# Performance work log

Measured on AMD Instinct MI355X. Metric: run time of the kernel, lower is better.

Reference implementation:

```python
import jax, jax.numpy as jnp
import numpy as np

B_, S_, D_ = 16, 2048, 256
H_ = 2 * D_          # S4D d_model = 2*hidden
NS = 64              # S4D state size (d_state)


def _layernorm(x, g, b, eps=1e-5):
    m = jnp.mean(x, axis=-1, keepdims=True)
    v = jnp.var(x, axis=-1, keepdims=True)
    return (x - m) * jax.lax.rsqrt(v + eps) * g + b


def setup_inputs() -> dict:
    key = jax.random.key(0)
    ks = jax.random.split(key, 12)
    x = jax.random.normal(ks[0], (B_, S_, D_), jnp.float32)
    # right-padded mask with varied lengths (signal: lengths = sum(mask), count_zeros = S - lengths)
    lengths = jax.random.randint(ks[1], (B_,), S_ // 2, S_ + 1)
    input_mask = (jnp.arange(S_)[None, :] < lengths[:, None]).astype(jnp.float32)
    # S4D (diag, diag-inv init, bilinear disc) parameters
    log_dt = jax.random.uniform(ks[2], (H_,), minval=jnp.log(1e-3), maxval=jnp.log(1e-1))
    log_A_real = jnp.log(0.5 * jnp.ones((H_, NS), jnp.float32))
    a_imag_row = (NS / jnp.pi) * (NS / (2.0 * jnp.arange(NS, dtype=jnp.float32) + 1.0) - 1.0)
    A_imag = jnp.broadcast_to(a_imag_row, (H_, NS)).copy()
    B_re = jnp.ones((H_, NS), jnp.float32)
    B_im = jnp.zeros((H_, NS), jnp.float32)
    C_re = jax.random.normal(ks[3], (H_, NS), jnp.float32) * (0.5 ** 0.5)
    C_im = jax.random.normal(ks[4], (H_, NS), jnp.float32) * (0.5 ** 0.5)
    D_skip = jax.random.normal(ks[5], (H_,), jnp.float32)
    # GLU: Linear(2D, 2D) then GLU -> D
    W_glu = jax.random.normal(ks[6], (2 * D_, 2 * D_), jnp.float32) / np.sqrt(2 * D_)
    b_glu = jnp.zeros((2 * D_,), jnp.float32)
    ln_gamma = jnp.ones((D_,), jnp.float32)
    ln_beta = jnp.zeros((D_,), jnp.float32)
    return {"input": x, "input_mask": input_mask, "log_dt": log_dt, "log_A_real": log_A_real,
            "A_imag": A_imag, "B_re": B_re, "B_im": B_im, "C_re": C_re, "C_im": C_im,
            "D_skip": D_skip, "W_glu": W_glu, "b_glu": b_glu, "ln_gamma": ln_gamma, "ln_beta": ln_beta}


def _s4d(z, log_dt, log_A_real, A_imag, B_re, B_im, C_re, C_im, D_skip):
    # z: [N, S, H] (transposed=False). Diagonal SSM, bilinear discretization, causal FFT conv.
    N, S, H = z.shape
    dt = jnp.exp(log_dt)[:, None]                        # [H,1]
    A = -jnp.exp(log_A_real) + 1j * A_imag               # [H,NS]
    Bc = B_re + 1j * B_im
    Cc = C_re + 1j * C_im
    dtA = dt * A
    dA = (1.0 + dtA / 2.0) / (1.0 - dtA / 2.0)           # bilinear
    Ct = Cc * Bc * dt / (1.0 - dtA / 2.0)                # folded B*C with bilinear dB factor
    # Vandermonde kernel K[h,l] = 2 Re sum_n Ct[h,n] * dA[h,n]^l
    vand = jnp.exp(jnp.log(dA)[:, :, None] * jnp.arange(S, dtype=jnp.float32))  # [H,NS,S] complex
    K = 2.0 * jnp.real(jnp.einsum('hn,hnl->hl', Ct, vand))                       # [H,S]
    L2 = 2 * S
    k_f = jnp.fft.rfft(K, n=L2)                          # [H, L2/2+1]
    x_f = jnp.fft.rfft(z, n=L2, axis=1)                  # [N, L2/2+1, H]
    y = jnp.fft.irfft(x_f * k_f.T[None], n=L2, axis=1)[:, :S, :]
    y = y + z * D_skip
    return jax.nn.gelu(y)                                # S4 block post-SSM activation; final_act=None, dropout=eval


def reference(input, input_mask, log_dt, log_A_real, A_imag, B_re, B_im, C_re, C_im,
              D_skip, W_glu, b_glu, ln_gamma, ln_beta):
    x = input
    N, S, D = x.shape
    res = x
    state = _layernorm(x, ln_gamma, ln_beta)             # prenorm=True
    count_zeros = jnp.sum(1.0 - input_mask, axis=1).astype(jnp.int32)   # [N]
    # reverse(state, cz): out[i] = state[(S-1-i-cz) mod S]  (flip then roll by count_zeros)
    rev_idx = (S - 1 - jnp.arange(S)[None, :] - count_zeros[:, None]) % S  # [N,S]
    reverse_bstate = jnp.take_along_axis(state, rev_idx[..., None], axis=1)
    z = jnp.concatenate([state, reverse_bstate], axis=-1)                 # [N,S,2D]
    z = _s4d(z, log_dt, log_A_real, A_imag, B_re, B_im, C_re, C_im, D_skip)
    fstate = z[..., :D]
    bstate = jnp.take_along_axis(z[..., D:], rev_idx[..., None], axis=1)  # reverse is an involution
    z = jnp.concatenate([fstate, bstate], axis=-1)                        # [N,S,2D]
    g = z @ W_glu + b_glu
    a, b = jnp.split(g, 2, axis=-1)
    out = a * jax.nn.sigmoid(b)                                           # GLU -> [N,S,D]
    out = out + res
    return out
```

## Files before the change

### kernel.cpp

```cpp
#include <hip/hip_runtime.h>
#include <hip/hip_bf16.h>
#include <math.h>

#define B_ 16
#define S_ 2048
#define D_ 256
#define H_ 512
#define NS_ 64
#define N2 4096
#define M_ (B_*S_)
#define XP(i) ((i) + ((i) >> 4))

typedef float f32x4 __attribute__((ext_vector_type(4)));
typedef short bf16x8 __attribute__((ext_vector_type(8)));

__device__ __forceinline__ unsigned short f2bf(float x) {
    __hip_bfloat16 h = __float2bfloat16(x);
    return *reinterpret_cast<unsigned short*>(&h);
}

__device__ __forceinline__ float gelu_f(float y) {
    float u = y + 0.044715f*y*y*y;
    return y / (1.0f + __builtin_exp2f(-2.3022082f * u));
}

__device__ __forceinline__ float cos_rev(float r) { return __builtin_amdgcn_cosf(r); }
__device__ __forceinline__ float sin_rev(float r) { return __builtin_amdgcn_sinf(r); }

template<bool INV, int MODE>
__device__ __forceinline__ void dft16(float* xr, float* xi) {
    const float SGN = INV ? 1.0f : -1.0f;
    constexpr float W16R[4][4] = {
        {1.f, 1.f, 1.f, 1.f},
        {1.f,  0.92387953251128674f,  0.70710678118654757f,  0.38268343236508984f},
        {1.f,  0.70710678118654757f,  0.0f,                 -0.70710678118654746f},
        {1.f,  0.38268343236508984f, -0.70710678118654746f, -0.92387953251128674f}};
    constexpr float W16I[4][4] = {
        {0.f, 0.f, 0.f, 0.f},
        {0.f, -0.38268343236508978f, -0.70710678118654746f, -0.92387953251128674f},
        {0.f, -0.70710678118654746f, -1.0f,                 -0.70710678118654757f},
        {0.f, -0.92387953251128674f, -0.70710678118654757f,  0.38268343236508967f}};
    float tr[16], ti[16];
    #pragma unroll
    for (int n0 = 0; n0 < 4; ++n0) {
        if (MODE == 1) {
            float ar = xr[n0],   ai = xi[n0];
            float br = xr[n0+4], bi = xi[n0+4];
            tr[0*4+n0] = ar + br;        ti[0*4+n0] = ai + bi;
            tr[2*4+n0] = ar - br;        ti[2*4+n0] = ai - bi;
            tr[1*4+n0] = ar - SGN*bi;    ti[1*4+n0] = ai + SGN*br;
            tr[3*4+n0] = ar + SGN*bi;    ti[3*4+n0] = ai - SGN*br;
        } else {
            float ar = xr[n0],    ai = xi[n0];
            float br = xr[n0+4],  bi = xi[n0+4];
            float cr = xr[n0+8],  ci = xi[n0+8];
            float dr = xr[n0+12], di = xi[n0+12];
            float sacr = ar+cr, saci = ai+ci;
            float dacr = ar-cr, daci = ai-ci;
            float sbdr = br+dr, sbdi = bi+di;
            float dbdr = br-dr, dbdi = bi-di;
            tr[0*4+n0] = sacr + sbdr;      ti[0*4+n0] = saci + sbdi;
            tr[2*4+n0] = sacr - sbdr;      ti[2*4+n0] = saci - sbdi;
            tr[1*4+n0] = dacr - SGN*dbdi;  ti[1*4+n0] = daci + SGN*dbdr;
            tr[3*4+n0] = dacr + SGN*dbdi;  ti[3*4+n0] = daci - SGN*dbdr;
        }
    }
    #pragma unroll
    for (int kl = 1; kl < 4; ++kl) {
        #pragma unroll
        for (int n0 = 1; n0 < 4; ++n0) {
            float wr = W16R[kl][n0];
            float wi = INV ? -W16I[kl][n0] : W16I[kl][n0];
            float pr = tr[kl*4+n0], pi = ti[kl*4+n0];
            tr[kl*4+n0] = pr*wr - pi*wi;
            ti[kl*4+n0] = pr*wi + pi*wr;
        }
    }
    #pragma unroll
    for (int kl = 0; kl < 4; ++kl) {
        float ar = tr[kl*4+0], ai = ti[kl*4+0];
        float br = tr[kl*4+1], bi = ti[kl*4+1];
        float cr = tr[kl*4+2], ci = ti[kl*4+2];
        float dr = tr[kl*4+3], di = ti[kl*4+3];
        float sacr = ar+cr, saci = ai+ci;
        float dacr = ar-cr, daci = ai-ci;
        float sbdr = br+dr, sbdi = bi+di;
        float dbdr = br-dr, dbdi = bi-di;
        xr[kl+0]  = sacr + sbdr;      xi[kl+0]  = saci + sbdi;
        xr[kl+4]  = dacr - SGN*dbdi;  xi[kl+4]  = daci + SGN*dbdr;
        if (MODE != 2) {
            xr[kl+8]  = sacr - sbdr;      xi[kl+8]  = saci - sbdi;
            xr[kl+12] = dacr + SGN*dbdi;  xi[kl+12] = daci - SGN*dbdr;
        }
    }
}

__device__ __forceinline__ void cmul(float& xr_, float& xi_, float wr, float wi) {
    float pr = xr_, pi = xi_;
    xr_ = pr*wr - pi*wi;
    xi_ = pr*wi + pi*wr;
}

__device__ __forceinline__ void twiddle_apply(float* xr, float* xi, float w1r, float w1i) {
    float w2r = w1r*w1r - w1i*w1i, w2i = 2.0f*w1r*w1i;
    float w4r = w2r*w2r - w2i*w2i, w4i = 2.0f*w2r*w2i;
    float w8r = w4r*w4r - w4i*w4i, w8i = 2.0f*w4r*w4i;
    float w3r = w2r*w1r - w2i*w1i, w3i = w2r*w1i + w2i*w1r;
    float w5r = w4r*w1r - w4i*w1i, w5i = w4r*w1i + w4i*w1r;
    float w6r = w4r*w2r - w4i*w2i, w6i = w4r*w2i + w4i*w2r;
    float w7r = w4r*w3r - w4i*w3i, w7i = w4r*w3i + w4i*w3r;
    cmul(xr[1],  xi[1],  w1r, w1i);
    cmul(xr[2],  xi[2],  w2r, w2i);
    cmul(xr[3],  xi[3],  w3r, w3i);
    cmul(xr[4],  xi[4],  w4r, w4i);
    cmul(xr[5],  xi[5],  w5r, w5i);
    cmul(xr[6],  xi[6],  w6r, w6i);
    cmul(xr[7],  xi[7],  w7r, w7i);
    cmul(xr[8],  xi[8],  w8r, w8i);
    float wr, wi;
    wr = w8r*w1r - w8i*w1i; wi = w8r*w1i + w8i*w1r; cmul(xr[9],  xi[9],  wr, wi);
    wr = w8r*w2r - w8i*w2i; wi = w8r*w2i + w8i*w2r; cmul(xr[10], xi[10], wr, wi);
    wr = w8r*w3r - w8i*w3i; wi = w8r*w3i + w8i*w3r; cmul(xr[11], xi[11], wr, wi);
    wr = w8r*w4r - w8i*w4i; wi = w8r*w4i + w8i*w4r; cmul(xr[12], xi[12], wr, wi);
    wr = w8r*w5r - w8i*w5i; wi = w8r*w5i + w8i*w5r; cmul(xr[13], xi[13], wr, wi);
    wr = w8r*w6r - w8i*w6i; wi = w8r*w6i + w8i*w6r; cmul(xr[14], xi[14], wr, wi);
    wr = w8r*w7r - w8i*w7i; wi = w8r*w7i + w8i*w7r; cmul(xr[15], xi[15], wr, wi);
}

__device__ __forceinline__ void fft4096_fwd_reg(float* xr, float* xi, float* lre, float* lim, int t) {
    dft16<false, 1>(xr, xi);
    float rv = (float)t * (1.0f/4096.0f);
    float w1r = cos_rev(rv), w1i = -sin_rev(rv);
    twiddle_apply(xr, xi, w1r, w1i);
    #pragma unroll
    for (int k = 0; k < 16; ++k) { int idx = XP(k*256 + t); lre[idx] = xr[k]; lim[idx] = xi[k]; }
    __syncthreads();
    int k1 = t >> 4, n3 = t & 15;
    #pragma unroll
    for (int n2 = 0; n2 < 16; ++n2) {
        int idx = XP(k1*256 + n2*16 + n3);
        xr[n2] = lre[idx]; xi[n2] = lim[idx];
    }
    dft16<false, 0>(xr, xi);
    rv = (float)n3 * (1.0f/256.0f);
    w1r = cos_rev(rv); w1i = -sin_rev(rv);
    twiddle_apply(xr, xi, w1r, w1i);
    __syncthreads();
    #pragma unroll
    for (int k = 0; k < 16; ++k) { int idx = XP(k1*256 + k*16 + n3); lre[idx] = xr[k]; lim[idx] = xi[k]; }
    __syncthreads();
    int k2 = t & 15;
    #pragma unroll
    for (int n3b = 0; n3b < 16; ++n3b) {
        int idx = XP(k1*256 + k2*16 + n3b);
        xr[n3b] = lre[idx]; xi[n3b] = lim[idx];
    }
    dft16<false, 0>(xr, xi);
}

__device__ __forceinline__ void fft4096_inv_reg(float* xr, float* xi, float* lre, float* lim, int t) {
    int k1 = t >> 4, k2 = t & 15;
    dft16<true, 0>(xr, xi);
    float rv = (float)k2 * (1.0f/256.0f);
    float w1r = cos_rev(rv), w1i = sin_rev(rv);
    twiddle_apply(xr, xi, w1r, w1i);
    __syncthreads();
    #pragma unroll
    for (int k = 0; k < 16; ++k) { int idx = XP(k1*256 + k2*16 + k); lre[idx] = xr[k]; lim[idx] = xi[k]; }
    __syncthreads();
    int n3 = t & 15;
    #pragma unroll
    for (int c = 0; c < 16; ++c) {
        int idx = XP(k1*256 + c*16 + n3);
        xr[c] = lre[idx]; xi[c] = lim[idx];
    }
    dft16<true, 0>(xr, xi);
    __syncthreads();
    #pragma unroll
    for (int k = 0; k < 16; ++k) { int idx = XP(k1*256 + k*16 + n3); lre[idx] = xr[k]; lim[idx] = xi[k]; }
    __syncthreads();
    #pragma unroll
    for (int k = 0; k < 16; ++k) {
        int idx = XP(k*256 + t);
        xr[k] = lre[idx]; xi[k] = lim[idx];
    }
    rv = (float)t * (1.0f/4096.0f);
    w1r = cos_rev(rv); w1i = sin_rev(rv);
    twiddle_apply(xr, xi, w1r, w1i);
    dft16<true, 2>(xr, xi);
}

__global__ void count_kernel(const float* __restrict__ mask, int* __restrict__ cz) {
    int b = blockIdx.x;
    int t = threadIdx.x;
    float s = 0.0f;
    for (int j = t; j < S_; j += 256) s += 1.0f - mask[b*S_ + j];
    for (int off = 32; off; off >>= 1) s += __shfl_xor(s, off);
    __shared__ float red[4];
    if ((t & 63) == 0) red[t >> 6] = s;
    __syncthreads();
    if (t == 0) {
        float tot = red[0] + red[1] + red[2] + red[3];
        cz[b] = (int)(tot + 0.5f);
    }
}

__global__ void wprep_kernel(const float* __restrict__ W, unsigned short* __restrict__ Wt) {
    int idx = blockIdx.x * 256 + threadIdx.x;
    int n = idx >> 9, k = idx & 511;
    Wt[idx] = f2bf(W[k*H_ + n]);
}

__global__ __launch_bounds__(256) void kfft_kernel(
        const float* __restrict__ log_dt, const float* __restrict__ log_A_real,
        const float* __restrict__ A_imag,
        const float* __restrict__ B_re, const float* __restrict__ B_im,
        const float* __restrict__ C_re, const float* __restrict__ C_im,
        float4* __restrict__ Kout) {
    int hp = blockIdx.x, t = threadIdx.x;
    int h0 = hp * 2;
    __shared__ float lre[N2 + N2/16];
    __shared__ float lim[N2 + N2/16];
    __shared__ float thrv[2][NS_], lnr2[2][NS_], ctr[2][NS_], cti[2][NS_];
    __shared__ float stpr[2][NS_], stpi[2][NS_];

    if (t < 128) {
        int ch = t >> 6, n = t & 63, h = h0 + ch;
        float dt = expf(log_dt[h]);
        float Ar = -expf(log_A_real[h*NS_ + n]);
        float Ai = A_imag[h*NS_ + n];
        float drr = 1.0f - 0.5f*dt*Ar, dii = -0.5f*dt*Ai;
        float nr = 1.0f + 0.5f*dt*Ar, ni =  0.5f*dt*Ai;
        float den = drr*drr + dii*dii;
        float dAr = (nr*drr + ni*dii) / den;
        float dAi = (ni*drr - nr*dii) / den;
        float cr = C_re[h*NS_+n], ci = C_im[h*NS_+n];
        float br = B_re[h*NS_+n], bi = B_im[h*NS_+n];
        float pr = (cr*br - ci*bi) * dt, pi = (cr*bi + ci*br) * dt;
        float qr = (pr*drr + pi*dii) / den;
        float qi = (pi*drr - pr*dii) / den;
        float trv = atan2f(dAi, dAr) * 0.15915494309189535f;
        float l2  = 0.5f * log2f(dAr*dAr + dAi*dAi);
        thrv[ch][n] = trv; lnr2[ch][n] = l2;
        ctr[ch][n] = qr;   cti[ch][n] = qi;
        float ms = __builtin_exp2f(l2 * 256.0f);
        float rv = trv * 256.0f; rv -= floorf(rv);
        stpr[ch][n] = ms * cos_rev(rv);
        stpi[ch][n] = ms * sin_rev(rv);
    }
    __syncthreads();

    float xr[16], xi[16];
    #pragma unroll
    for (int j = 0; j < 16; ++j) { xr[j] = 0.0f; xi[j] = 0.0f; }

    float tf = (float)t;
    #pragma unroll
    for (int ch = 0; ch < 2; ++ch) {
        for (int n = 0; n < NS_; ++n) {
            float trv = thrv[ch][n], l2 = lnr2[ch][n];
            float f = trv * tf; f -= floorf(f);
            float mag = __builtin_exp2f(l2 * tf);
            float vr = mag * cos_rev(f);
            float vi = mag * sin_rev(f);
            float sr = stpr[ch][n], si = stpi[ch][n];
            float cr = ctr[ch][n],  ci = cti[ch][n];
            #pragma unroll
            for (int j = 0; j < 8; ++j) {
                float contrib = cr*vr - ci*vi;
                if (ch == 0) xr[j] += contrib; else xi[j] += contrib;
                float nvr = vr*sr - vi*si;
                vi = vr*si + vi*sr;
                vr = nvr;
            }
        }
    }
    #pragma unroll
    for (int j = 0; j < 8; ++j) { xr[j] *= 2.0f; xi[j] *= 2.0f; }

    fft4096_fwd_reg(xr, xi, lre, lim, t);

    __syncthreads();
    #pragma unroll
    for (int k = 0; k < 16; ++k) { int idx = XP(k*256 + t); lre[idx] = xr[k]; lim[idx] = xi[k]; }
    __syncthreads();

    const float scale = 1.0f / (float)N2;
    #pragma unroll
    for (int it = 0; it < 16; ++it) {
        int j = 256*it + t;
        int k = (t >> 4) + ((t & 15) << 4) + (it << 8);
        int kc = (N2 - k) & (N2 - 1);
        int j2 = ((kc >> 8) << 8) + ((kc & 15) << 4) + ((kc >> 4) & 15);
        float za = xr[it], zb = xi[it];
        float zc = lre[XP(j2)], zd = lim[XP(j2)];
        float Xr = 0.5f*(za + zc), Xi2 = 0.5f*(zb - zd);
        float Yr = 0.5f*(zb + zd), Yi = 0.5f*(zc - za);
        Kout[(size_t)hp*N2 + j] = make_float4(Xr*scale, Xi2*scale, Yr*scale, Yi*scale);
    }
}

__global__ __launch_bounds__(256) void ln_kernel(
        const float* __restrict__ x, const float* __restrict__ gamma,
        const float* __restrict__ beta, float* __restrict__ zf) {
    int blk = blockIdx.x;
    int b = blk >> 6;
    int s0 = (blk & 63) * 32;
    int t = threadIdx.x;
    int lane = t & 63, wave = t >> 6;
    __shared__ float st[32][257];

    float4 g4  = *(const float4*)(gamma + lane*4);
    float4 be4 = *(const float4*)(beta  + lane*4);
    for (int q = 0; q < 8; ++q) {
        int row = wave*8 + q;
        int s = s0 + row;
        float4 v = *(const float4*)(x + ((size_t)(b*S_ + s))*D_ + lane*4);
        float sum = v.x + v.y + v.z + v.w;
        float ss  = v.x*v.x + v.y*v.y + v.z*v.z + v.w*v.w;
        for (int off = 32; off; off >>= 1) {
            sum += __shfl_xor(sum, off);
            ss  += __shfl_xor(ss, off);
        }
        float mean = sum * (1.0f/(float)D_);
        float var  = ss  * (1.0f/(float)D_) - mean*mean;
        float rstd = rsqrtf(var + 1e-5f);
        st[row][lane*4+0] = (v.x - mean)*rstd*g4.x + be4.x;
        st[row][lane*4+1] = (v.y - mean)*rstd*g4.y + be4.y;
        st[row][lane*4+2] = (v.z - mean)*rstd*g4.z + be4.z;
        st[row][lane*4+3] = (v.w - mean)*rstd*g4.w + be4.w;
    }
    __syncthreads();
    int s_off = t & 31, dg = t >> 5;
    int s = s0 + s_off;
    for (int i = 0; i < 32; ++i) {
        int d = dg + 8*i;
        zf[((size_t)(b*D_ + d))*S_ + s] = st[s_off][d];
    }
}

__global__ __launch_bounds__(256) void fftconv_kernel(
        const float* __restrict__ zf, const float4* __restrict__ Kf4,
        const float* __restrict__ D_skip, const int* __restrict__ cz,
        unsigned short* __restrict__ ybf) {
    int blk = blockIdx.x;
    int b  = blk >> 8;
    int hp = blk & 255;
    int h0 = hp * 2;
    int t = threadIdx.x;
    __shared__ float lre[N2 + N2/16];
    __shared__ float lim[N2 + N2/16];

    bool back = (h0 >= D_);
    int czb = cz[b];
    const float* zrow1 = zf + ((size_t)(b*D_ + (h0 & (D_-1))))*S_;
    const float* zrow2 = zrow1 + S_;

    float xr[16], xi[16];
    float z1r[8], z2r[8];
    #pragma unroll
    for (int j = 0; j < 8; ++j) {
        int s = t + 256*j;
        int p = s;
        if (back) { p = 2*S_ - 1 - czb - s; if (p >= S_) p -= S_; }
        float v1 = zrow1[p], v2 = zrow2[p];
        z1r[j] = v1; z2r[j] = v2;
        xr[j] = v1;  xi[j] = v2;
        xr[j+8] = 0.0f; xi[j+8] = 0.0f;
    }

    fft4096_fwd_reg(xr, xi, lre, lim, t);

    __syncthreads();
    #pragma unroll
    for (int k = 0; k < 16; ++k) { int idx = XP(k*256 + t); lre[idx] = xr[k]; lim[idx] = xi[k]; }
    __syncthreads();

    const float4* kp = Kf4 + (size_t)hp * N2;
    #pragma unroll
    for (int it = 0; it < 16; ++it) {
        int j = 256*it + t;
        int k = (t >> 4) + ((t & 15) << 4) + (it << 8);
        int kc = (N2 - k) & (N2 - 1);
        int j2 = ((kc >> 8) << 8) + ((kc & 15) << 4) + ((kc >> 4) & 15);
        float za = xr[it], zb = xi[it];
        float zc = lre[XP(j2)], zd = lim[XP(j2)];
        float Xr = 0.5f*(za + zc), Xi2 = 0.5f*(zb - zd);
        float Yr = 0.5f*(zb + zd), Yi = 0.5f*(zc - za);
        float4 kk = kp[j];
        float Pr = Xr*kk.x - Xi2*kk.y, Pi = Xr*kk.y + Xi2*kk.x;
        float Qr = Yr*kk.z - Yi*kk.w,  Qi = Yr*kk.w + Yi*kk.z;
        xr[it] = Pr - Qi;
        xi[it] = Pi + Qr;
    }

    fft4096_inv_reg(xr, xi, lre, lim, t);

    float dsk1 = D_skip[h0], dsk2 = D_skip[h0+1];
    unsigned short* yb1 = ybf + ((size_t)(b*H_ + h0    ))*S_;
    unsigned short* yb2 = ybf + ((size_t)(b*H_ + h0 + 1))*S_;
    #pragma unroll
    for (int j = 0; j < 8; ++j) {
        int s = t + 256*j;
        float y1 = xr[j] + dsk1 * z1r[j];
        float y2 = xi[j] + dsk2 * z2r[j];
        yb1[s] = f2bf(gelu_f(y1));
        yb2[s] = f2bf(gelu_f(y2));
    }
}

__global__ __launch_bounds__(256) void transpose_kernel(
        const unsigned short* __restrict__ ybf, const int* __restrict__ cz,
        unsigned short* __restrict__ A) {
    int b  = blockIdx.z;
    int h0 = blockIdx.y * 64;
    int s0 = blockIdx.x * 64;
    int t = threadIdx.x;
    int tx = t & 63, ty = t >> 6;
    __shared__ unsigned short tile[64][65];
    bool back = (h0 >= D_);
    int czb = cz[b];
    int s = s0 + tx;
    int scol = back ? ((2*S_ - 1 - czb - s) % S_) : s;
    for (int i = 0; i < 16; ++i) {
        int hh = ty*16 + i;
        tile[hh][tx] = ybf[((size_t)(b*H_ + h0 + hh))*S_ + scol];
    }
    __syncthreads();
    for (int i = 0; i < 16; ++i) {
        int sl = ty*16 + i;
        A[((size_t)(b*S_ + s0 + sl))*H_ + h0 + tx] = tile[tx][sl];
    }
}

__global__ __launch_bounds__(256) void glu_gemm_kernel(
        const unsigned short* __restrict__ A, const unsigned short* __restrict__ Wt,
        const float* __restrict__ bglu, const float* __restrict__ x,
        float* __restrict__ out) {
    int m0 = blockIdx.x * 128;
    int nh = blockIdx.y;
    int t = threadIdx.x;
    int lane = t & 63, w = t >> 6;
    __shared__ __align__(16) unsigned short Ab[2][4096];
    __shared__ __align__(16) unsigned short Bb[2][8192];

    f32x4 acc[2][16];
    #pragma unroll
    for (int mf = 0; mf < 2; ++mf)
        #pragma unroll
        for (int nf = 0; nf < 16; ++nf)
            acc[mf][nf] = (f32x4){0.0f, 0.0f, 0.0f, 0.0f};

    int r = t >> 2;
    int kch = (t & 3) * 8;
    int wbase = (t >> 6) * 1024;

    auto stage = [&](int buf, int kk) {
        #pragma unroll
        for (int i = 0; i < 2; ++i) {
            int row = i*64 + r;
            int kel = kch ^ (((row >> 2) & 3) << 3);
            const unsigned short* src = A + ((size_t)(m0 + row))*H_ + kk + kel;
            char* dst = (char*)&Ab[buf][0] + i*4096 + wbase;
            __builtin_amdgcn_global_load_lds((const __attribute__((address_space(1))) void*)src,
                                             (__attribute__((address_space(3))) void*)dst, 16, 0, 0);
        }
        #pragma unroll
        for (int i = 0; i < 4; ++i) {
            int rb = i*64 + r;
            int n = nh*128 + rb + (rb & 128);
            int kel = kch ^ (((rb >> 2) & 3) << 3);
            const unsigned short* src = Wt + ((size_t)n)*H_ + kk + kel;
            char* dst = (char*)&Bb[buf][0] + i*4096 + wbase;
            __builtin_amdgcn_global_load_lds((const __attribute__((address_space(1))) void*)src,
                                             (__attribute__((address_space(3))) void*)dst, 16, 0, 0);
        }
    };

    int lr = lane & 15, ksel = lane >> 4;
    stage(0, 0);
    __syncthreads();

    #pragma unroll 1
    for (int step = 0; step < 16; ++step) {
        int cur = step & 1;
        if (step < 15) stage(cur ^ 1, (step + 1) * 32);
        const char* pa = (const char*)&Ab[cur][0];
        const char* pb = (const char*)&Bb[cur][0];
        bf16x8 af[2];
        #pragma unroll
        for (int mf = 0; mf < 2; ++mf) {
            int arow = w*32 + mf*16 + lr;
            af[mf] = *(const bf16x8*)(pa + arow*64 + ((ksel*16) ^ (((arow >> 2) & 3) << 4)));
        }
        #pragma unroll
        for (int nf = 0; nf < 16; ++nf) {
            int brow = nf*16 + lr;
            bf16x8 bv = *(const bf16x8*)(pb + brow*64 + ((ksel*16) ^ (((brow >> 2) & 3) << 4)));
            acc[0][nf] = __builtin_amdgcn_mfma_f32_16x16x32_bf16(af[0], bv, acc[0][nf], 0, 0, 0);
            acc[1][nf] = __builtin_amdgcn_mfma_f32_16x16x32_bf16(af[1], bv, acc[1][nf], 0, 0, 0);
        }
        __syncthreads();
    }

    int r4 = (lane >> 4) * 4;
    #pragma unroll
    for (int mf = 0; mf < 2; ++mf) {
        #pragma unroll
        for (int nf = 0; nf < 8; ++nf) {
            int tc = nf*16 + lr;
            int dcol = nh*128 + tc;
            float ba = bglu[dcol];
            float bb = bglu[256 + dcol];
            #pragma unroll
            for (int rr = 0; rr < 4; ++rr) {
                int row = w*32 + mf*16 + r4 + rr;
                size_t mi = (size_t)(m0 + row);
                float av = acc[mf][nf][rr] + ba;
                float bv = acc[mf][nf+8][rr] + bb;
                float sig = 1.0f / (1.0f + __builtin_exp2f(-1.4426950408889634f * bv));
                out[mi*D_ + dcol] = av*sig + x[mi*D_ + dcol];
            }
        }
    }
}

extern "C" void kernel_launch(void* const* d_in, const int* in_sizes, int n_in,
                              void* d_out, int out_size, void* d_ws, size_t ws_size,
                              hipStream_t stream) {
    const float* x         = (const float*)d_in[0];
    const float* mask      = (const float*)d_in[1];
    const float* log_dt    = (const float*)d_in[2];
    const float* log_A_real= (const float*)d_in[3];
    const float* A_imag    = (const float*)d_in[4];
    const float* B_re      = (const float*)d_in[5];
    const float* B_im      = (const float*)d_in[6];
    const float* C_re      = (const float*)d_in[7];
    const float* C_im      = (const float*)d_in[8];
    const float* D_skip    = (const float*)d_in[9];
    const float* W_glu     = (const float*)d_in[10];
    const float* b_glu     = (const float*)d_in[11];
    const float* ln_gamma  = (const float*)d_in[12];
    const float* ln_beta   = (const float*)d_in[13];
    float* out = (float*)d_out;

    char* ws = (char*)d_ws;
    int*            cz  = (int*)ws;
    float*          zf  = (float*)(ws + 256);
    unsigned short* ybf = (unsigned short*)(ws + 256 + 33554432);
    float4*         Kf  = (float4*)(ws + 256 + 67108864);
    unsigned short* Abf = (unsigned short*)(ws + 256 + 83886080);
    unsigned short* Wt  = (unsigned short*)(ws + 256 + 117440512);

    count_kernel<<<B_, 256, 0, stream>>>(mask, cz);
    wprep_kernel<<<(H_*H_)/256, 256, 0, stream>>>(W_glu, Wt);
    kfft_kernel<<<H_/2, 256, 0, stream>>>(log_dt, log_A_real, A_imag, B_re, B_im, C_re, C_im, Kf);
    ln_kernel<<<B_*(S_/32), 256, 0, stream>>>(x, ln_gamma, ln_beta, zf);
    fftconv_kernel<<<B_*(H_/2), 256, 0, stream>>>(zf, (const float4*)Kf, D_skip, cz, ybf);
    transpose_kernel<<<dim3(S_/64, H_/64, B_), 256, 0, stream>>>(ybf, cz, Abf);
    glu_gemm_kernel<<<dim3(M_/128, 2), 256, 0, stream>>>(Abf, Wt, b_glu, x, out);
}
```

Baseline: 306.4 us.

## Interleave FFT LDS as float2, prefetch kernel spectrum, tile weight transpose

The separate real and imaginary LDS arrays used by the FFT stages become one interleaved float2 array, so each exchange issues a single 64-bit LDS access instead of two 32-bit ones. The fftconv kernel now loads the precomputed kernel spectrum into registers in two halves, issued around the LDS write and barrier, so the global-load latency overlaps the exchange. The weight-prep transpose now goes through a 64x64 shared-memory tile so both reads and writes are coalesced. The float2 layout with the same padding may change bank-conflict behaviour, and the prefetch adds register pressure.

```diff
diff --git a/kernel.cpp b/kernel.cpp
--- a/kernel.cpp
+++ b/kernel.cpp
@@ -9,7 +9,7 @@
 #define NS_ 64
 #define N2 4096
 #define M_ (B_*S_)
-#define XP(i) ((i) + ((i) >> 4))
+#define XP2(i) ((i) + ((i) >> 4))
 
 typedef float f32x4 __attribute__((ext_vector_type(4)));
 typedef short bf16x8 __attribute__((ext_vector_type(8)));
@@ -127,19 +127,19 @@
     wr = w8r*w7r - w8i*w7i; wi = w8r*w7i + w8i*w7r; cmul(xr[15], xi[15], wr, wi);
 }
 
-__device__ __forceinline__ void fft4096_fwd_reg(float* xr, float* xi, float* lre, float* lim, int t) {
+__device__ __forceinline__ void fft4096_fwd_reg(float* xr, float* xi, float2* ld, int t) {
     dft16<false, 1>(xr, xi);
     float rv = (float)t * (1.0f/4096.0f);
     float w1r = cos_rev(rv), w1i = -sin_rev(rv);
     twiddle_apply(xr, xi, w1r, w1i);
     #pragma unroll
-    for (int k = 0; k < 16; ++k) { int idx = XP(k*256 + t); lre[idx] = xr[k]; lim[idx] = xi[k]; }
+    for (int k = 0; k < 16; ++k) ld[XP2(k*256 + t)] = make_float2(xr[k], xi[k]);
     __syncthreads();
     int k1 = t >> 4, n3 = t & 15;
     #pragma unroll
     for (int n2 = 0; n2 < 16; ++n2) {
-        int idx = XP(k1*256 + n2*16 + n3);
-        xr[n2] = lre[idx]; xi[n2] = lim[idx];
+        float2 v = ld[XP2(k1*256 + n2*16 + n3)];
+        xr[n2] = v.x; xi[n2] = v.y;
     }
     dft16<false, 0>(xr, xi);
     rv = (float)n3 * (1.0f/256.0f);
@@ -147,18 +147,18 @@
     twiddle_apply(xr, xi, w1r, w1i);
     __syncthreads();
     #pragma unroll
-    for (int k = 0; k < 16; ++k) { int idx = XP(k1*256 + k*16 + n3); lre[idx] = xr[k]; lim[idx] = xi[k]; }
+    for (int k = 0; k < 16; ++k) ld[XP2(k1*256 + k*16 + n3)] = make_float2(xr[k], xi[k]);
     __syncthreads();
     int k2 = t & 15;
     #pragma unroll
     for (int n3b = 0; n3b < 16; ++n3b) {
-        int idx = XP(k1*256 + k2*16 + n3b);
-        xr[n3b] = lre[idx]; xi[n3b] = lim[idx];
+        float2 v = ld[XP2(k1*256 + k2*16 + n3b)];
+        xr[n3b] = v.x; xi[n3b] = v.y;
     }
     dft16<false, 0>(xr, xi);
 }
 
-__device__ __forceinline__ void fft4096_inv_reg(float* xr, float* xi, float* lre, float* lim, int t) {
+__device__ __forceinline__ void fft4096_inv_reg(float* xr, float* xi, float2* ld, int t) {
     int k1 = t >> 4, k2 = t & 15;
     dft16<true, 0>(xr, xi);
     float rv = (float)k2 * (1.0f/256.0f);
@@ -166,23 +166,23 @@
     twiddle_apply(xr, xi, w1r, w1i);
     __syncthreads();
     #pragma unroll
-    for (int k = 0; k < 16; ++k) { int idx = XP(k1*256 + k2*16 + k); lre[idx] = xr[k]; lim[idx] = xi[k]; }
+    for (int k = 0; k < 16; ++k) ld[XP2(k1*256 + k2*16 + k)] = make_float2(xr[k], xi[k]);
     __syncthreads();
     int n3 = t & 15;
     #pragma unroll
     for (int c = 0; c < 16; ++c) {
-        int idx = XP(k1*256 + c*16 + n3);
-        xr[c] = lre[idx]; xi[c] = lim[idx];
+        float2 v = ld[XP2(k1*256 + c*16 + n3)];
+        xr[c] = v.x; xi[c] = v.y;
     }
     dft16<true, 0>(xr, xi);
     __syncthreads();
     #pragma unroll
-    for (int k = 0; k < 16; ++k) { int idx = XP(k1*256 + k*16 + n3); lre[idx] = xr[k]; lim[idx] = xi[k]; }
+    for (int k = 0; k < 16; ++k) ld[XP2(k1*256 + k*16 + n3)] = make_float2(xr[k], xi[k]);
     __syncthreads();
     #pragma unroll
     for (int k = 0; k < 16; ++k) {
-        int idx = XP(k*256 + t);
-        xr[k] = lre[idx]; xi[k] = lim[idx];
+        float2 v = ld[XP2(k*256 + t)];
+        xr[k] = v.x; xi[k] = v.y;
     }
     rv = (float)t * (1.0f/4096.0f);
     w1r = cos_rev(rv); w1i = sin_rev(rv);
@@ -205,10 +205,24 @@
     }
 }
 
-__global__ void wprep_kernel(const float* __restrict__ W, unsigned short* __restrict__ Wt) {
-    int idx = blockIdx.x * 256 + threadIdx.x;
-    int n = idx >> 9, k = idx & 511;
-    Wt[idx] = f2bf(W[k*H_ + n]);
+__global__ __launch_bounds__(256) void wprep_kernel(const float* __restrict__ W,
+                                                    unsigned short* __restrict__ Wt) {
+    int n0 = (blockIdx.x & 7) * 64;
+    int k0 = (blockIdx.x >> 3) * 64;
+    int t = threadIdx.x;
+    int tx = t & 63, ty = t >> 6;
+    __shared__ float tile[64][65];
+    #pragma unroll
+    for (int i = 0; i < 16; ++i) {
+        int krow = ty*16 + i;
+        tile[krow][tx] = W[(size_t)(k0 + krow)*H_ + n0 + tx];
+    }
+    __syncthreads();
+    #pragma unroll
+    for (int i = 0; i < 16; ++i) {
+        int nrow = ty*16 + i;
+        Wt[(size_t)(n0 + nrow)*H_ + k0 + tx] = f2bf(tile[tx][nrow]);
+    }
 }
 
 __global__ __launch_bounds__(256) void kfft_kernel(
@@ -219,8 +233,7 @@
         float4* __restrict__ Kout) {
     int hp = blockIdx.x, t = threadIdx.x;
     int h0 = hp * 2;
-    __shared__ float lre[N2 + N2/16];
-    __shared__ float lim[N2 + N2/16];
+    __shared__ float2 ld[N2 + N2/16];
     __shared__ float thrv[2][NS_], lnr2[2][NS_], ctr[2][NS_], cti[2][NS_];
     __shared__ float stpr[2][NS_], stpi[2][NS_];
 
@@ -278,11 +291,11 @@
     #pragma unroll
     for (int j = 0; j < 8; ++j) { xr[j] *= 2.0f; xi[j] *= 2.0f; }
 
-    fft4096_fwd_reg(xr, xi, lre, lim, t);
-
-    __syncthreads();
-    #pragma unroll
-    for (int k = 0; k < 16; ++k) { int idx = XP(k*256 + t); lre[idx] = xr[k]; lim[idx] = xi[k]; }
+    fft4096_fwd_reg(xr, xi, ld, t);
+
+    __syncthreads();
+    #pragma unroll
+    for (int k = 0; k < 16; ++k) ld[XP2(k*256 + t)] = make_float2(xr[k], xi[k]);
     __syncthreads();
 
     const float scale = 1.0f / (float)N2;
@@ -293,7 +306,8 @@
         int kc = (N2 - k) & (N2 - 1);
         int j2 = ((kc >> 8) << 8) + ((kc & 15) << 4) + ((kc >> 4) & 15);
         float za = xr[it], zb = xi[it];
-        float zc = lre[XP(j2)], zd = lim[XP(j2)];
+        float2 v2 = ld[XP2(j2)];
+        float zc = v2.x, zd = v2.y;
         float Xr = 0.5f*(za + zc), Xi2 = 0.5f*(zb - zd);
         float Yr = 0.5f*(zb + zd), Yi = 0.5f*(zc - za);
         Kout[(size_t)hp*N2 + j] = make_float4(Xr*scale, Xi2*scale, Yr*scale, Yi*scale);
@@ -348,8 +362,7 @@
     int hp = blk & 255;
     int h0 = hp * 2;
     int t = threadIdx.x;
-    __shared__ float lre[N2 + N2/16];
-    __shared__ float lim[N2 + N2/16];
+    __shared__ float2 ld[N2 + N2/16];
 
     bool back = (h0 >= D_);
     int czb = cz[b];
@@ -369,32 +382,62 @@
         xr[j+8] = 0.0f; xi[j+8] = 0.0f;
     }
 
-    fft4096_fwd_reg(xr, xi, lre, lim, t);
-
-    __syncthreads();
-    #pragma unroll
-    for (int k = 0; k < 16; ++k) { int idx = XP(k*256 + t); lre[idx] = xr[k]; lim[idx] = xi[k]; }
-    __syncthreads();
+    fft4096_fwd_reg(xr, xi, ld, t);
 
     const float4* kp = Kf4 + (size_t)hp * N2;
-    #pragma unroll
-    for (int it = 0; it < 16; ++it) {
-        int j = 256*it + t;
-        int k = (t >> 4) + ((t & 15) << 4) + (it << 8);
-        int kc = (N2 - k) & (N2 - 1);
-        int j2 = ((kc >> 8) << 8) + ((kc & 15) << 4) + ((kc >> 4) & 15);
+    float4 kk0[8];
+    #pragma unroll
+    for (int it = 0; it < 8; ++it) kk0[it] = kp[256*it + t];
+
+    __syncthreads();
+    #pragma unroll
+    for (int k = 0; k < 16; ++k) ld[XP2(k*256 + t)] = make_float2(xr[k], xi[k]);
+    __syncthreads();
+
+    float4 kk1[8];
+    #pragma unroll
+    for (int it = 0; it < 8; ++it) kk1[it] = kp[256*(8 + it) + t];
+
+    #pragma unroll
+    for (int it = 0; it < 8; ++it) {
+        int j2;
+        {
+            int k = (t >> 4) + ((t & 15) << 4) + (it << 8);
+            int kc = (N2 - k) & (N2 - 1);
+            j2 = ((kc >> 8) << 8) + ((kc & 15) << 4) + ((kc >> 4) & 15);
+        }
         float za = xr[it], zb = xi[it];
-        float zc = lre[XP(j2)], zd = lim[XP(j2)];
+        float2 v2 = ld[XP2(j2)];
+        float zc = v2.x, zd = v2.y;
         float Xr = 0.5f*(za + zc), Xi2 = 0.5f*(zb - zd);
         float Yr = 0.5f*(zb + zd), Yi = 0.5f*(zc - za);
-        float4 kk = kp[j];
+        float4 kk = kk0[it];
         float Pr = Xr*kk.x - Xi2*kk.y, Pi = Xr*kk.y + Xi2*kk.x;
         float Qr = Yr*kk.z - Yi*kk.w,  Qi = Yr*kk.w + Yi*kk.z;
         xr[it] = Pr - Qi;
         xi[it] = Pi + Qr;
     }
-
-    fft4096_inv_reg(xr, xi, lre, lim, t);
+    #pragma unroll
+    for (int it = 8; it < 16; ++it) {
+        int j2;
+        {
+            int k = (t >> 4) + ((t & 15) << 4) + (it << 8);
+            int kc = (N2 - k) & (N2 - 1);
+            j2 = ((kc >> 8) << 8) + ((kc & 15) << 4) + ((kc >> 4) & 15);
+        }
+        float za = xr[it], zb = xi[it];
+        float2 v2 = ld[XP2(j2)];
+        float zc = v2.x, zd = v2.y;
+        float Xr = 0.5f*(za + zc), Xi2 = 0.5f*(zb - zd);
+        float Yr = 0.5f*(zb + zd), Yi = 0.5f*(zc - za);
+        float4 kk = kk1[it - 8];
+        float Pr = Xr*kk.x - Xi2*kk.y, Pi = Xr*kk.y + Xi2*kk.x;
+        float Qr = Yr*kk.z - Yi*kk.w,  Qi = Yr*kk.w + Yi*kk.z;
+        xr[it] = Pr - Qi;
+        xi[it] = Pi + Qr;
+    }
+
+    fft4096_inv_reg(xr, xi, ld, t);
 
     float dsk1 = D_skip[h0], dsk2 = D_skip[h0+1];
     unsigned short* yb1 = ybf + ((size_t)(b*H_ + h0    ))*S_;
@@ -553,7 +596,7 @@
     unsigned short* Wt  = (unsigned short*)(ws + 256 + 117440512);
 
     count_kernel<<<B_, 256, 0, stream>>>(mask, cz);
-    wprep_kernel<<<(H_*H_)/256, 256, 0, stream>>>(W_glu, Wt);
+    wprep_kernel<<<64, 256, 0, stream>>>(W_glu, Wt);
     kfft_kernel<<<H_/2, 256, 0, stream>>>(log_dt, log_A_real, A_imag, B_re, B_im, C_re, C_im, Kf);
     ln_kernel<<<B_*(S_/32), 256, 0, stream>>>(x, ln_gamma, ln_beta, zf);
     fftconv_kernel<<<B_*(H_/2), 256, 0, stream>>>(zf, (const float4*)Kf, D_skip, cz, ybf);
```

New measurement: 286.4 us. 6.5% less time.
